# Kernel optimization log

Measured on AMD Instinct MI355X. Metric: run time of the kernel, lower is better.

Reference implementation:

```python
import jax, jax.numpy as jnp
import numpy as np

TEMPERATURE = 0.8
TOP_P = 0.9
NEG_INF = float('-inf')


def _top_k_filter(logits, k):
    # keep only the top-k logits per row; mask the rest to -inf.
    # torch.topk + scatter mask == threshold at the k-th largest value (ties measure-zero for float logits)
    kth = jax.lax.top_k(logits, k)[0][..., -1:]  # [B, 1]
    return jnp.where(logits < kth, NEG_INF, logits)


def _top_p_filter(logits, p):
    # nucleus filtering: sort desc, cumulative softmax mass, drop tail past p (always keep the top token)
    B, V = logits.shape
    order = jnp.argsort(-logits, axis=-1)                       # [B, V] descending order
    sorted_logits = jnp.take_along_axis(logits, order, axis=-1)
    cdf = jnp.cumsum(jax.nn.softmax(sorted_logits, axis=-1), axis=-1)
    remove_sorted = cdf > p
    remove_sorted = jnp.roll(remove_sorted, 1, axis=-1).at[..., 0].set(False)  # shift so first token crossing p is kept
    rows = jnp.arange(B)[:, None]
    remove = jnp.zeros((B, V), dtype=bool).at[rows, order].set(remove_sorted)  # scatter back to original positions
    return jnp.where(remove, NEG_INF, logits)


def _sample_multinomial(probs, key):
    # inverse-CDF sampling: idx = #{cumsum <= r}
    r = jax.random.uniform(key, (probs.shape[0], 1), dtype=probs.dtype)
    cdf = jnp.cumsum(probs, axis=-1)
    return jnp.sum(cdf <= r, axis=-1, keepdims=True)  # [B, 1] int


def setup_inputs() -> dict:
    key = jax.random.key(0)
    logits = jax.random.normal(key, (256, 50257), dtype=jnp.float32) * 4.0
    return {"logits": logits, "top_k": 50}


def reference(logits, top_k):
    logits = logits / TEMPERATURE
    logits = _top_k_filter(logits, top_k)
    logits = _top_p_filter(logits, TOP_P)
    probs = jax.nn.softmax(logits, axis=-1)
    next_ids = _sample_multinomial(probs, jax.random.fold_in(jax.random.key(0), 1))
    return next_ids
```

## Files before the change

### kernel.cpp

```cpp
#include <hip/hip_runtime.h>
#include <stdint.h>


#define BLOCK 512
#define BINS  4096
#define CAP   1024
#define TOPP  0.9f

__device__ __forceinline__ unsigned orderKey(float x) {
  unsigned u = __float_as_uint(x);
  return (u & 0x80000000u) ? ~u : (u | 0x80000000u);
}

__device__ __forceinline__ void threefry2x32(unsigned k0, unsigned k1,
                                             unsigned x0, unsigned x1,
                                             unsigned &o0, unsigned &o1) {
  unsigned k2 = k0 ^ k1 ^ 0x1BD11BDAu;
  x0 += k0; x1 += k1;
#define TFR(rr) { x0 += x1; x1 = (x1 << (rr)) | (x1 >> (32 - (rr))); x1 ^= x0; }
  TFR(13) TFR(15) TFR(26) TFR(6)
  x0 += k1; x1 += k2 + 1u;
  TFR(17) TFR(29) TFR(16) TFR(24)
  x0 += k2; x1 += k0 + 2u;
  TFR(13) TFR(15) TFR(26) TFR(6)
  x0 += k0; x1 += k1 + 3u;
  TFR(17) TFR(29) TFR(16) TFR(24)
  x0 += k1; x1 += k2 + 4u;
  TFR(13) TFR(15) TFR(26) TFR(6)
  x0 += k2; x1 += k0 + 5u;
#undef TFR
  o0 = x0; o1 = x1;
}

__global__ __launch_bounds__(BLOCK) void Sampler_28845000360542_kernel(
    const float* __restrict__ logits, const int* __restrict__ topk_ptr,
    int* __restrict__ out, int V, int B) {
  __shared__ unsigned hist[BINS];
  __shared__ float    cval[CAP];
  __shared__ int      cidx[CAP];
  __shared__ float    sval[CAP];
  __shared__ int      sidx[CAP];
  __shared__ unsigned psum[BLOCK];
  __shared__ short    ord[CAP];
  __shared__ unsigned s_cnt;
  __shared__ int      s_binLo;
  __shared__ int      s_ns;
  __shared__ int      s_K;
  __shared__ float    s_S2;
  __shared__ float    s_r;

  const int tid = threadIdx.x;
  const int row = blockIdx.x;
  const float* __restrict__ rp = logits + (size_t)row * (size_t)V;
  const float4* __restrict__ rp4 = (const float4*)rp;
  const int V4 = V >> 2;

  int k = topk_ptr[0];
  if (k < 1) k = 1;
  if (k > V) k = V;

  for (int i = tid; i < BINS; i += BLOCK) hist[i] = 0u;
  if (tid == 0) s_cnt = 0u;
  __syncthreads();

  for (int i = tid; i < V4; i += BLOCK) {
    float4 v = rp4[i];
    atomicAdd(&hist[orderKey(v.x) >> 20], 1u);
    atomicAdd(&hist[orderKey(v.y) >> 20], 1u);
    atomicAdd(&hist[orderKey(v.z) >> 20], 1u);
    atomicAdd(&hist[orderKey(v.w) >> 20], 1u);
  }
  for (int i = (V4 << 2) + tid; i < V; i += BLOCK)
    atomicAdd(&hist[orderKey(rp[i]) >> 20], 1u);
  __syncthreads();

  {
    const int C = BINS / BLOCK;
    unsigned s = 0;
#pragma unroll
    for (int j = 0; j < C; ++j) s += hist[tid * C + j];
    psum[tid] = s;
  }
  __syncthreads();

  if (tid == 0) {
    const int C = BINS / BLOCK;
    unsigned cum = 0;
    int chunk = 0;
    for (int t = BLOCK - 1; t >= 0; --t) {
      if (cum + psum[t] >= (unsigned)k) { chunk = t; break; }
      cum += psum[t];
    }
    int bstar = chunk * C;
    for (int b = chunk * C + C - 1; b >= chunk * C; --b) {
      if (cum + hist[b] >= (unsigned)k) { bstar = b; break; }
      cum += hist[b];
    }
    unsigned nCol = cum + hist[bstar];
    int bLo = bstar;
    if (bstar > 0 && nCol + hist[bstar - 1] <= (unsigned)CAP) bLo = bstar - 1;
    s_binLo = bLo;
  }
  __syncthreads();

  const unsigned binLo = (unsigned)s_binLo;
  for (int i = tid; i < V4; i += BLOCK) {
    float4 v = rp4[i];
    float vv[4] = {v.x, v.y, v.z, v.w};
#pragma unroll
    for (int c = 0; c < 4; ++c) {
      if ((orderKey(vv[c]) >> 20) >= binLo) {
        unsigned pos = atomicAdd(&s_cnt, 1u);
        if (pos < CAP) { cval[pos] = vv[c]; cidx[pos] = (i << 2) + c; }
      }
    }
  }
  for (int i = (V4 << 2) + tid; i < V; i += BLOCK) {
    float x = rp[i];
    if ((orderKey(x) >> 20) >= binLo) {
      unsigned pos = atomicAdd(&s_cnt, 1u);
      if (pos < CAP) { cval[pos] = x; cidx[pos] = i; }
    }
  }
  __syncthreads();

  int n = (int)s_cnt;
  if (n > CAP) n = CAP;

  for (int i = tid; i < n; i += BLOCK) cval[i] = cval[i] / 0.8f;
  __syncthreads();
  for (int i = tid; i < n; i += BLOCK) {
    float v = cval[i];
    int   id = cidx[i];
    int   rk = 0;
    for (int j = 0; j < n; ++j) {
      float vj = cval[j];
      rk += (vj > v) || (vj == v && cidx[j] < id);
    }
    sval[rk] = v;
    sidx[rk] = id;
  }
  __syncthreads();

  if (tid == 0) {
    int ns = (n < k) ? n : k;
    float kv = sval[ns - 1];
    while (ns < n && sval[ns] == kv) ++ns;
    s_ns = ns;
  }
  __syncthreads();
  const int ns = s_ns;

  const float m = sval[0];
  for (int i = tid; i < ns; i += BLOCK) cval[i] = expf(sval[i] - m);
  __syncthreads();

  if (tid == 0) {
    float S = 0.f;
    for (int i = 0; i < ns; ++i) S += cval[i];
    float c = 0.f;
    int K = ns;
    for (int i = 0; i < ns; ++i) {
      if (i > 0 && c > TOPP) { K = i; break; }
      c += cval[i] / S;
    }
    float S2 = 0.f;
    for (int i = 0; i < K; ++i) S2 += cval[i];
    s_K = K;
    s_S2 = S2;

    unsigned kk0, kk1, o0, o1;
    threefry2x32(0u, 0u, 0u, 1u, kk0, kk1);
    threefry2x32(kk0, kk1, 0u, (unsigned)row, o0, o1);
    unsigned bits = o0 ^ o1;
    float r = __uint_as_float((bits >> 9) | 0x3F800000u) - 1.0f;
    s_r = (r < 0.f) ? 0.f : r;
    (void)B;
  }
  __syncthreads();
  const int K = s_K;

  for (int i = tid; i < K; i += BLOCK) {
    int id = sidx[i];
    int rk = 0;
    for (int j = 0; j < K; ++j) rk += (sidx[j] < id);
    ord[rk] = (short)i;
  }
  __syncthreads();

  if (tid == 0) {
    const float S2 = s_S2;
    const float rr = s_r;
    float c = 0.f;
    int ans = V;
    for (int t = 0; t < K; ++t) {
      int i = ord[t];
      c += cval[i] / S2;
      if (c > rr) { ans = sidx[i]; break; }
    }
    out[row] = ans;
  }
}

extern "C" void kernel_launch(void* const* d_in, const int* in_sizes, int n_in,
                              void* d_out, int out_size, void* d_ws, size_t ws_size,
                              hipStream_t stream) {
  const float* logits = (const float*)d_in[0];
  const int*   topk   = (const int*)d_in[1];
  int*         out    = (int*)d_out;
  const int B = out_size;
  const int V = in_sizes[0] / B;
  hipLaunchKernelGGL(Sampler_28845000360542_kernel, dim3(B), dim3(BLOCK), 0,
                     stream, logits, topk, out, V, B);
}
```

Before: 118.5 us.

## Split per-row sampler into multi-kernel pipeline with chunked histogram and collect

```diff
diff --git a/kernel.cpp b/kernel.cpp
--- a/kernel.cpp
+++ b/kernel.cpp
@@ -2,10 +2,12 @@
 #include <stdint.h>
 
 
-#define BLOCK 512
-#define BINS  4096
-#define CAP   1024
-#define TOPP  0.9f
+#define BINS     4096
+#define CAP      1024
+#define TOPP     0.9f
+#define S_CHUNKS 8
+#define HBLOCK   256
+#define TAILB    512
 
 __device__ __forceinline__ unsigned orderKey(float x) {
   unsigned u = __float_as_uint(x);
@@ -32,104 +34,154 @@
   o0 = x0; o1 = x1;
 }
 
-__global__ __launch_bounds__(BLOCK) void Sampler_28845000360542_kernel(
-    const float* __restrict__ logits, const int* __restrict__ topk_ptr,
-    int* __restrict__ out, int V, int B) {
+__global__ __launch_bounds__(256) void k_zero(unsigned* __restrict__ p, int n) {
+  int i = blockIdx.x * 256 + threadIdx.x;
+  int stride = gridDim.x * 256;
+  for (; i < n; i += stride) p[i] = 0u;
+}
+
+__global__ __launch_bounds__(HBLOCK) void k_hist(
+    const float* __restrict__ logits, unsigned* __restrict__ ghist, int V) {
   __shared__ unsigned hist[BINS];
-  __shared__ float    cval[CAP];
-  __shared__ int      cidx[CAP];
-  __shared__ float    sval[CAP];
-  __shared__ int      sidx[CAP];
-  __shared__ unsigned psum[BLOCK];
-  __shared__ short    ord[CAP];
-  __shared__ unsigned s_cnt;
-  __shared__ int      s_binLo;
-  __shared__ int      s_ns;
-  __shared__ int      s_K;
-  __shared__ float    s_S2;
-  __shared__ float    s_r;
-
-  const int tid = threadIdx.x;
-  const int row = blockIdx.x;
+  const int row = blockIdx.y, chunk = blockIdx.x, tid = threadIdx.x;
   const float* __restrict__ rp = logits + (size_t)row * (size_t)V;
   const float4* __restrict__ rp4 = (const float4*)rp;
   const int V4 = V >> 2;
-
-  int k = topk_ptr[0];
-  if (k < 1) k = 1;
-  if (k > V) k = V;
-
-  for (int i = tid; i < BINS; i += BLOCK) hist[i] = 0u;
-  if (tid == 0) s_cnt = 0u;
-  __syncthreads();
-
-  for (int i = tid; i < V4; i += BLOCK) {
+  const int beg = (int)((long long)chunk * V4 / S_CHUNKS);
+  const int end = (int)((long long)(chunk + 1) * V4 / S_CHUNKS);
+
+  for (int i = tid; i < BINS; i += HBLOCK) hist[i] = 0u;
+  __syncthreads();
+
+  for (int i = beg + tid; i < end; i += HBLOCK) {
     float4 v = rp4[i];
     atomicAdd(&hist[orderKey(v.x) >> 20], 1u);
     atomicAdd(&hist[orderKey(v.y) >> 20], 1u);
     atomicAdd(&hist[orderKey(v.z) >> 20], 1u);
     atomicAdd(&hist[orderKey(v.w) >> 20], 1u);
   }
-  for (int i = (V4 << 2) + tid; i < V; i += BLOCK)
-    atomicAdd(&hist[orderKey(rp[i]) >> 20], 1u);
-  __syncthreads();
-
-  {
-    const int C = BINS / BLOCK;
-    unsigned s = 0;
+  if (chunk == S_CHUNKS - 1) {
+    for (int i = (V4 << 2) + tid; i < V; i += HBLOCK)
+      atomicAdd(&hist[orderKey(rp[i]) >> 20], 1u);
+  }
+  __syncthreads();
+
+  unsigned* __restrict__ gh = ghist + (size_t)row * BINS;
+  for (int i = tid; i < BINS; i += HBLOCK) {
+    unsigned c = hist[i];
+    if (c) atomicAdd(&gh[i], c);
+  }
+}
+
+__global__ __launch_bounds__(256) void k_select(
+    const unsigned* __restrict__ ghist, const int* __restrict__ topk_ptr,
+    int* __restrict__ binLoArr, int V) {
+  __shared__ unsigned hist[BINS];
+  __shared__ unsigned psum[256];
+  const int row = blockIdx.x, tid = threadIdx.x;
+  const unsigned* __restrict__ gh = ghist + (size_t)row * BINS;
+  for (int i = tid; i < BINS; i += 256) hist[i] = gh[i];
+  __syncthreads();
+
+  int k = topk_ptr[0];
+  if (k < 1) k = 1;
+  if (k > V) k = V;
+
+  const int C = BINS / 256;
+  unsigned s = 0;
 #pragma unroll
-    for (int j = 0; j < C; ++j) s += hist[tid * C + j];
-    psum[tid] = s;
-  }
-  __syncthreads();
-
-  if (tid == 0) {
-    const int C = BINS / BLOCK;
+  for (int j = 0; j < C; ++j) s += hist[tid * C + j];
+  psum[tid] = s;
+  __syncthreads();
+
+  if (tid == 0) {
     unsigned cum = 0;
-    int chunk = 0;
-    for (int t = BLOCK - 1; t >= 0; --t) {
-      if (cum + psum[t] >= (unsigned)k) { chunk = t; break; }
+    int ch = 0;
+    for (int t = 255; t >= 0; --t) {
+      if (cum + psum[t] >= (unsigned)k) { ch = t; break; }
       cum += psum[t];
     }
-    int bstar = chunk * C;
-    for (int b = chunk * C + C - 1; b >= chunk * C; --b) {
+    int bstar = ch * C;
+    for (int b = ch * C + C - 1; b >= ch * C; --b) {
       if (cum + hist[b] >= (unsigned)k) { bstar = b; break; }
       cum += hist[b];
     }
     unsigned nCol = cum + hist[bstar];
     int bLo = bstar;
     if (bstar > 0 && nCol + hist[bstar - 1] <= (unsigned)CAP) bLo = bstar - 1;
-    s_binLo = bLo;
-  }
-  __syncthreads();
-
-  const unsigned binLo = (unsigned)s_binLo;
-  for (int i = tid; i < V4; i += BLOCK) {
+    binLoArr[row] = bLo;
+  }
+}
+
+__global__ __launch_bounds__(HBLOCK) void k_collect(
+    const float* __restrict__ logits, const int* __restrict__ binLoArr,
+    unsigned* __restrict__ cnt, float* __restrict__ cvalg,
+    int* __restrict__ cidxg, int V) {
+  const int row = blockIdx.y, chunk = blockIdx.x, tid = threadIdx.x;
+  const unsigned binLo = (unsigned)binLoArr[row];
+  const float* __restrict__ rp = logits + (size_t)row * (size_t)V;
+  const float4* __restrict__ rp4 = (const float4*)rp;
+  const int V4 = V >> 2;
+  const int beg = (int)((long long)chunk * V4 / S_CHUNKS);
+  const int end = (int)((long long)(chunk + 1) * V4 / S_CHUNKS);
+  float* __restrict__ cv = cvalg + (size_t)row * CAP;
+  int*   __restrict__ ci = cidxg + (size_t)row * CAP;
+
+  for (int i = beg + tid; i < end; i += HBLOCK) {
     float4 v = rp4[i];
     float vv[4] = {v.x, v.y, v.z, v.w};
 #pragma unroll
     for (int c = 0; c < 4; ++c) {
       if ((orderKey(vv[c]) >> 20) >= binLo) {
-        unsigned pos = atomicAdd(&s_cnt, 1u);
-        if (pos < CAP) { cval[pos] = vv[c]; cidx[pos] = (i << 2) + c; }
+        unsigned pos = atomicAdd(&cnt[row], 1u);
+        if (pos < CAP) { cv[pos] = vv[c]; ci[pos] = (i << 2) + c; }
       }
     }
   }
-  for (int i = (V4 << 2) + tid; i < V; i += BLOCK) {
-    float x = rp[i];
-    if ((orderKey(x) >> 20) >= binLo) {
-      unsigned pos = atomicAdd(&s_cnt, 1u);
-      if (pos < CAP) { cval[pos] = x; cidx[pos] = i; }
-    }
-  }
-  __syncthreads();
-
-  int n = (int)s_cnt;
+  if (chunk == S_CHUNKS - 1) {
+    for (int i = (V4 << 2) + tid; i < V; i += HBLOCK) {
+      float x = rp[i];
+      if ((orderKey(x) >> 20) >= binLo) {
+        unsigned pos = atomicAdd(&cnt[row], 1u);
+        if (pos < CAP) { cv[pos] = x; ci[pos] = i; }
+      }
+    }
+  }
+}
+
+__global__ __launch_bounds__(TAILB) void k_tail(
+    const unsigned* __restrict__ cnt, const float* __restrict__ cvalg,
+    const int* __restrict__ cidxg, const int* __restrict__ topk_ptr,
+    int* __restrict__ out, int V) {
+  __shared__ float cval[CAP];
+  __shared__ int   cidx[CAP];
+  __shared__ float sval[CAP];
+  __shared__ int   sidx[CAP];
+  __shared__ short ord[CAP];
+  __shared__ int   s_ns;
+  __shared__ int   s_K;
+  __shared__ float s_S2;
+  __shared__ float s_r;
+
+  const int tid = threadIdx.x;
+  const int row = blockIdx.x;
+
+  int k = topk_ptr[0];
+  if (k < 1) k = 1;
+  if (k > V) k = V;
+
+  int n = (int)cnt[row];
   if (n > CAP) n = CAP;
 
-  for (int i = tid; i < n; i += BLOCK) cval[i] = cval[i] / 0.8f;
-  __syncthreads();
-  for (int i = tid; i < n; i += BLOCK) {
+  const float* __restrict__ cv = cvalg + (size_t)row * CAP;
+  const int*   __restrict__ ci = cidxg + (size_t)row * CAP;
+  for (int i = tid; i < n; i += TAILB) {
+    cval[i] = cv[i] / 0.8f;
+    cidx[i] = ci[i];
+  }
+  __syncthreads();
+
+  for (int i = tid; i < n; i += TAILB) {
     float v = cval[i];
     int   id = cidx[i];
     int   rk = 0;
@@ -152,7 +204,7 @@
   const int ns = s_ns;
 
   const float m = sval[0];
-  for (int i = tid; i < ns; i += BLOCK) cval[i] = expf(sval[i] - m);
+  for (int i = tid; i < ns; i += TAILB) cval[i] = expf(sval[i] - m);
   __syncthreads();
 
   if (tid == 0) {
@@ -175,12 +227,11 @@
     unsigned bits = o0 ^ o1;
     float r = __uint_as_float((bits >> 9) | 0x3F800000u) - 1.0f;
     s_r = (r < 0.f) ? 0.f : r;
-    (void)B;
   }
   __syncthreads();
   const int K = s_K;
 
-  for (int i = tid; i < K; i += BLOCK) {
+  for (int i = tid; i < K; i += TAILB) {
     int id = sidx[i];
     int rk = 0;
     for (int j = 0; j < K; ++j) rk += (sidx[j] < id);
@@ -210,6 +261,24 @@
   int*         out    = (int*)d_out;
   const int B = out_size;
   const int V = in_sizes[0] / B;
-  hipLaunchKernelGGL(Sampler_28845000360542_kernel, dim3(B), dim3(BLOCK), 0,
-                     stream, logits, topk, out, V, B);
-}
+
+  char* ws = (char*)d_ws;
+  unsigned* ghist  = (unsigned*)ws;
+  unsigned* cnt    = (unsigned*)(ws + (size_t)B * BINS * 4);
+  int*      binLo  = (int*)(ws + (size_t)B * BINS * 4 + B * 4);
+  float*    cvalg  = (float*)(ws + (size_t)B * BINS * 4 + B * 8);
+  int*      cidxg  = (int*)(ws + (size_t)B * BINS * 4 + B * 8 +
+                            (size_t)B * CAP * 4);
+
+  const int nzero = B * BINS + B;
+  hipLaunchKernelGGL(k_zero, dim3((nzero + 255) / 256), dim3(256), 0, stream,
+                     ghist, nzero);
+  hipLaunchKernelGGL(k_hist, dim3(S_CHUNKS, B), dim3(HBLOCK), 0, stream,
+                     logits, ghist, V);
+  hipLaunchKernelGGL(k_select, dim3(B), dim3(256), 0, stream,
+                     ghist, topk, binLo, V);
+  hipLaunchKernelGGL(k_collect, dim3(S_CHUNKS, B), dim3(HBLOCK), 0, stream,
+                     logits, binLo, cnt, cvalg, cidxg, V);
+  hipLaunchKernelGGL(k_tail, dim3(B), dim3(TAILB), 0, stream,
+                     cnt, cvalg, cidxg, topk, out, V);
+}
```

Result: slower. 160.6 us (+35.6%).

## Split each row across eight blocks with per-chunk candidate selection and merge kernel

Applied to the files above, without the earlier changes.

```diff
diff --git a/kernel.cpp b/kernel.cpp
--- a/kernel.cpp
+++ b/kernel.cpp
@@ -2,10 +2,13 @@
 #include <stdint.h>
 
 
-#define BLOCK 512
-#define BINS  4096
-#define CAP   1024
-#define TOPP  0.9f
+#define BINS     4096
+#define S_CHUNKS 8
+#define PB       256
+#define SEG      256
+#define CAPT     (S_CHUNKS * SEG)
+#define TB       512
+#define TOPP     0.9f
 
 __device__ __forceinline__ unsigned orderKey(float x) {
   unsigned u = __float_as_uint(x);
@@ -32,140 +35,222 @@
   o0 = x0; o1 = x1;
 }
 
-__global__ __launch_bounds__(BLOCK) void Sampler_28845000360542_kernel(
+__global__ __launch_bounds__(PB) void k_pass1(
     const float* __restrict__ logits, const int* __restrict__ topk_ptr,
-    int* __restrict__ out, int V, int B) {
+    int* __restrict__ scnt, float* __restrict__ svals, int* __restrict__ sidxs,
+    int V) {
   __shared__ unsigned hist[BINS];
-  __shared__ float    cval[CAP];
-  __shared__ int      cidx[CAP];
-  __shared__ float    sval[CAP];
-  __shared__ int      sidx[CAP];
-  __shared__ unsigned psum[BLOCK];
-  __shared__ short    ord[CAP];
-  __shared__ unsigned s_cnt;
-  __shared__ int      s_binLo;
-  __shared__ int      s_ns;
-  __shared__ int      s_K;
-  __shared__ float    s_S2;
-  __shared__ float    s_r;
-
-  const int tid = threadIdx.x;
-  const int row = blockIdx.x;
+  __shared__ unsigned psum[PB];
+  __shared__ float    lval[SEG];
+  __shared__ int      lidx[SEG];
+  __shared__ unsigned lcnt;
+  __shared__ int      s_b;
+
+  const int row = blockIdx.y, chunk = blockIdx.x, tid = threadIdx.x;
   const float* __restrict__ rp = logits + (size_t)row * (size_t)V;
   const float4* __restrict__ rp4 = (const float4*)rp;
   const int V4 = V >> 2;
-
-  int k = topk_ptr[0];
-  if (k < 1) k = 1;
-  if (k > V) k = V;
-
-  for (int i = tid; i < BINS; i += BLOCK) hist[i] = 0u;
-  if (tid == 0) s_cnt = 0u;
-  __syncthreads();
-
-  for (int i = tid; i < V4; i += BLOCK) {
+  const int beg = (int)((long long)chunk * V4 / S_CHUNKS);
+  const int end = (int)((long long)(chunk + 1) * V4 / S_CHUNKS);
+  const bool last = (chunk == S_CHUNKS - 1);
+  const int rembeg = V4 << 2;
+
+  for (int i = tid; i < BINS; i += PB) hist[i] = 0u;
+  if (tid == 0) lcnt = 0u;
+  __syncthreads();
+
+  for (int i = beg + tid; i < end; i += PB) {
     float4 v = rp4[i];
     atomicAdd(&hist[orderKey(v.x) >> 20], 1u);
     atomicAdd(&hist[orderKey(v.y) >> 20], 1u);
     atomicAdd(&hist[orderKey(v.z) >> 20], 1u);
     atomicAdd(&hist[orderKey(v.w) >> 20], 1u);
   }
-  for (int i = (V4 << 2) + tid; i < V; i += BLOCK)
-    atomicAdd(&hist[orderKey(rp[i]) >> 20], 1u);
-  __syncthreads();
-
+  if (last)
+    for (int i = rembeg + tid; i < V; i += PB)
+      atomicAdd(&hist[orderKey(rp[i]) >> 20], 1u);
+  __syncthreads();
+
+  int k = topk_ptr[0];
+  if (k < 1) k = 1;
+  if (k > V) k = V;
+  const int ec = (end - beg) * 4 + (last ? (V - rembeg) : 0);
+  if (k > ec) k = ec;
+
+  const int C = BINS / PB;
   {
-    const int C = BINS / BLOCK;
     unsigned s = 0;
 #pragma unroll
     for (int j = 0; j < C; ++j) s += hist[tid * C + j];
     psum[tid] = s;
   }
   __syncthreads();
-
-  if (tid == 0) {
-    const int C = BINS / BLOCK;
+  if (tid == 0) {
     unsigned cum = 0;
-    int chunk = 0;
-    for (int t = BLOCK - 1; t >= 0; --t) {
-      if (cum + psum[t] >= (unsigned)k) { chunk = t; break; }
+    int ch = 0;
+    for (int t = PB - 1; t >= 0; --t) {
+      if (cum + psum[t] >= (unsigned)k) { ch = t; break; }
       cum += psum[t];
     }
-    int bstar = chunk * C;
-    for (int b = chunk * C + C - 1; b >= chunk * C; --b) {
+    int bstar = ch * C;
+    for (int b = ch * C + C - 1; b >= ch * C; --b) {
       if (cum + hist[b] >= (unsigned)k) { bstar = b; break; }
       cum += hist[b];
     }
-    unsigned nCol = cum + hist[bstar];
-    int bLo = bstar;
-    if (bstar > 0 && nCol + hist[bstar - 1] <= (unsigned)CAP) bLo = bstar - 1;
-    s_binLo = bLo;
-  }
-  __syncthreads();
-
-  const unsigned binLo = (unsigned)s_binLo;
-  for (int i = tid; i < V4; i += BLOCK) {
+    s_b = (bstar > 0) ? bstar - 1 : 0;
+  }
+  __syncthreads();
+
+  const unsigned bLo = (unsigned)s_b;
+  for (int i = beg + tid; i < end; i += PB) {
     float4 v = rp4[i];
     float vv[4] = {v.x, v.y, v.z, v.w};
 #pragma unroll
     for (int c = 0; c < 4; ++c) {
-      if ((orderKey(vv[c]) >> 20) >= binLo) {
-        unsigned pos = atomicAdd(&s_cnt, 1u);
-        if (pos < CAP) { cval[pos] = vv[c]; cidx[pos] = (i << 2) + c; }
+      if ((orderKey(vv[c]) >> 20) >= bLo) {
+        unsigned pos = atomicAdd(&lcnt, 1u);
+        if (pos < SEG) { lval[pos] = vv[c]; lidx[pos] = (i << 2) + c; }
       }
     }
   }
-  for (int i = (V4 << 2) + tid; i < V; i += BLOCK) {
-    float x = rp[i];
-    if ((orderKey(x) >> 20) >= binLo) {
-      unsigned pos = atomicAdd(&s_cnt, 1u);
-      if (pos < CAP) { cval[pos] = x; cidx[pos] = i; }
-    }
-  }
-  __syncthreads();
-
-  int n = (int)s_cnt;
-  if (n > CAP) n = CAP;
-
-  for (int i = tid; i < n; i += BLOCK) cval[i] = cval[i] / 0.8f;
-  __syncthreads();
-  for (int i = tid; i < n; i += BLOCK) {
-    float v = cval[i];
-    int   id = cidx[i];
+  if (last)
+    for (int i = rembeg + tid; i < V; i += PB) {
+      float x = rp[i];
+      if ((orderKey(x) >> 20) >= bLo) {
+        unsigned pos = atomicAdd(&lcnt, 1u);
+        if (pos < SEG) { lval[pos] = x; lidx[pos] = i; }
+      }
+    }
+  __syncthreads();
+
+  int n = (lcnt > SEG) ? SEG : (int)lcnt;
+  const int sb = row * S_CHUNKS + chunk;
+  if (tid == 0) scnt[sb] = n;
+  float* __restrict__ ov = svals + (size_t)sb * SEG;
+  int*   __restrict__ oi = sidxs + (size_t)sb * SEG;
+  for (int i = tid; i < n; i += PB) { ov[i] = lval[i]; oi[i] = lidx[i]; }
+}
+
+__global__ __launch_bounds__(TB) void k_tail(
+    const int* __restrict__ scnt, const float* __restrict__ svals,
+    const int* __restrict__ sidxs, const int* __restrict__ topk_ptr,
+    int* __restrict__ out, int V) {
+  __shared__ float    cval[CAPT];
+  __shared__ int      cidx[CAPT];
+  __shared__ float    sval[CAPT];
+  __shared__ int      sidx[CAPT];
+  __shared__ short    ord[CAPT];
+  __shared__ unsigned hist[BINS];
+  __shared__ unsigned psum[TB];
+  __shared__ int      s_off[S_CHUNKS + 1];
+  __shared__ unsigned s_mc;
+  __shared__ int      s_bg, s_ns, s_K;
+  __shared__ float    s_S2, s_r;
+
+  const int row = blockIdx.x, tid = threadIdx.x;
+  int k = topk_ptr[0];
+  if (k < 1) k = 1;
+  if (k > V) k = V;
+
+  if (tid == 0) {
+    int off = 0;
+    for (int c = 0; c < S_CHUNKS; ++c) { s_off[c] = off; off += scnt[row * S_CHUNKS + c]; }
+    s_off[S_CHUNKS] = off;
+    s_mc = 0u;
+  }
+  for (int i = tid; i < BINS; i += TB) hist[i] = 0u;
+  __syncthreads();
+
+  const int n = s_off[S_CHUNKS];
+  for (int c = 0; c < S_CHUNKS; ++c) {
+    const int cn = s_off[c + 1] - s_off[c];
+    const int o  = s_off[c];
+    const float* __restrict__ sv = svals + (size_t)(row * S_CHUNKS + c) * SEG;
+    const int*   __restrict__ si = sidxs + (size_t)(row * S_CHUNKS + c) * SEG;
+    for (int i = tid; i < cn; i += TB) {
+      float x = sv[i];
+      cval[o + i] = x;
+      cidx[o + i] = si[i];
+      atomicAdd(&hist[orderKey(x) >> 20], 1u);
+    }
+  }
+  __syncthreads();
+
+  const int kk = (k > n) ? n : k;
+  {
+    const int C = BINS / TB;
+    unsigned s = 0;
+#pragma unroll
+    for (int j = 0; j < C; ++j) s += hist[tid * C + j];
+    psum[tid] = s;
+  }
+  __syncthreads();
+  if (tid == 0) {
+    const int C = BINS / TB;
+    unsigned cum = 0;
+    int ch = 0;
+    for (int t = TB - 1; t >= 0; --t) {
+      if (cum + psum[t] >= (unsigned)kk) { ch = t; break; }
+      cum += psum[t];
+    }
+    int bstar = ch * C;
+    for (int b = ch * C + C - 1; b >= ch * C; --b) {
+      if (cum + hist[b] >= (unsigned)kk) { bstar = b; break; }
+      cum += hist[b];
+    }
+    s_bg = (bstar > 0) ? bstar - 1 : 0;
+  }
+  __syncthreads();
+
+  const unsigned bg = (unsigned)s_bg;
+  for (int i = tid; i < n; i += TB) {
+    float x = cval[i];
+    if ((orderKey(x) >> 20) >= bg) {
+      unsigned pos = atomicAdd(&s_mc, 1u);
+      sval[pos] = x / 0.8f;
+      sidx[pos] = cidx[i];
+    }
+  }
+  __syncthreads();
+  const int m = (int)s_mc;
+
+  for (int i = tid; i < m; i += TB) {
+    float v = sval[i];
+    int   id = sidx[i];
     int   rk = 0;
-    for (int j = 0; j < n; ++j) {
-      float vj = cval[j];
-      rk += (vj > v) || (vj == v && cidx[j] < id);
-    }
-    sval[rk] = v;
-    sidx[rk] = id;
-  }
-  __syncthreads();
-
-  if (tid == 0) {
-    int ns = (n < k) ? n : k;
-    float kv = sval[ns - 1];
-    while (ns < n && sval[ns] == kv) ++ns;
+    for (int j = 0; j < m; ++j) {
+      float vj = sval[j];
+      rk += (vj > v) || (vj == v && sidx[j] < id);
+    }
+    cval[rk] = v;
+    cidx[rk] = id;
+  }
+  __syncthreads();
+
+  if (tid == 0) {
+    int ns = (m < kk) ? m : kk;
+    float kv = cval[ns - 1];
+    while (ns < m && cval[ns] == kv) ++ns;
     s_ns = ns;
   }
   __syncthreads();
   const int ns = s_ns;
 
-  const float m = sval[0];
-  for (int i = tid; i < ns; i += BLOCK) cval[i] = expf(sval[i] - m);
+  const float mx = cval[0];
+  for (int i = tid; i < ns; i += TB) sval[i] = expf(cval[i] - mx);
   __syncthreads();
 
   if (tid == 0) {
     float S = 0.f;
-    for (int i = 0; i < ns; ++i) S += cval[i];
+    for (int i = 0; i < ns; ++i) S += sval[i];
     float c = 0.f;
     int K = ns;
     for (int i = 0; i < ns; ++i) {
       if (i > 0 && c > TOPP) { K = i; break; }
-      c += cval[i] / S;
+      c += sval[i] / S;
     }
     float S2 = 0.f;
-    for (int i = 0; i < K; ++i) S2 += cval[i];
+    for (int i = 0; i < K; ++i) S2 += sval[i];
     s_K = K;
     s_S2 = S2;
 
@@ -175,15 +260,14 @@
     unsigned bits = o0 ^ o1;
     float r = __uint_as_float((bits >> 9) | 0x3F800000u) - 1.0f;
     s_r = (r < 0.f) ? 0.f : r;
-    (void)B;
   }
   __syncthreads();
   const int K = s_K;
 
-  for (int i = tid; i < K; i += BLOCK) {
-    int id = sidx[i];
+  for (int i = tid; i < K; i += TB) {
+    int id = cidx[i];
     int rk = 0;
-    for (int j = 0; j < K; ++j) rk += (sidx[j] < id);
+    for (int j = 0; j < K; ++j) rk += (cidx[j] < id);
     ord[rk] = (short)i;
   }
   __syncthreads();
@@ -195,8 +279,8 @@
     int ans = V;
     for (int t = 0; t < K; ++t) {
       int i = ord[t];
-      c += cval[i] / S2;
-      if (c > rr) { ans = sidx[i]; break; }
+      c += sval[i] / S2;
+      if (c > rr) { ans = cidx[i]; break; }
     }
     out[row] = ans;
   }
@@ -210,6 +294,15 @@
   int*         out    = (int*)d_out;
   const int B = out_size;
   const int V = in_sizes[0] / B;
-  hipLaunchKernelGGL(Sampler_28845000360542_kernel, dim3(B), dim3(BLOCK), 0,
-                     stream, logits, topk, out, V, B);
-}
+
+  char* ws = (char*)d_ws;
+  int*   scnt  = (int*)ws;
+  float* svals = (float*)(ws + (size_t)B * S_CHUNKS * 4);
+  int*   sidxs = (int*)(ws + (size_t)B * S_CHUNKS * 4 +
+                        (size_t)B * S_CHUNKS * SEG * 4);
+
+  hipLaunchKernelGGL(k_pass1, dim3(S_CHUNKS, B), dim3(PB), 0, stream,
+                     logits, topk, scnt, svals, sidxs, V);
+  hipLaunchKernelGGL(k_tail, dim3(B), dim3(TB), 0, stream,
+                     scnt, svals, sidxs, topk, out, V);
+}
```

Result: slower. 135.3 us (+14.2%).

## Single-pass fixed-threshold prefilter with wave-level top-k selection and fallback path

Applied to the files above, without the earlier changes.

```diff
diff --git a/kernel.cpp b/kernel.cpp
--- a/kernel.cpp
+++ b/kernel.cpp
@@ -2,10 +2,13 @@
 #include <stdint.h>
 
 
-#define BLOCK 512
-#define BINS  4096
-#define CAP   1024
-#define TOPP  0.9f
+#define BLOCK  1024
+#define CAPN   2048
+#define SLOTS  (CAPN / 64)
+#define WCAP   256
+#define TOPP   0.9f
+#define TOPT_F 8.0f
+#define OK8    0xC1000000u
 
 __device__ __forceinline__ unsigned orderKey(float x) {
   unsigned u = __float_as_uint(x);
@@ -32,24 +35,23 @@
   o0 = x0; o1 = x1;
 }
 
-__global__ __launch_bounds__(BLOCK) void Sampler_28845000360542_kernel(
+__global__ __launch_bounds__(BLOCK) void k_all(
     const float* __restrict__ logits, const int* __restrict__ topk_ptr,
-    int* __restrict__ out, int V, int B) {
-  __shared__ unsigned hist[BINS];
-  __shared__ float    cval[CAP];
-  __shared__ int      cidx[CAP];
-  __shared__ float    sval[CAP];
-  __shared__ int      sidx[CAP];
-  __shared__ unsigned psum[BLOCK];
-  __shared__ short    ord[CAP];
-  __shared__ unsigned s_cnt;
-  __shared__ int      s_binLo;
-  __shared__ int      s_ns;
-  __shared__ int      s_K;
-  __shared__ float    s_S2;
-  __shared__ float    s_r;
-
-  const int tid = threadIdx.x;
+    int* __restrict__ out, int V) {
+  __shared__ float    bufv[CAPN];
+  __shared__ int      bufi[CAPN];
+  __shared__ float    wv[WCAP];
+  __shared__ int      wi[WCAP];
+  __shared__ float    sv[WCAP];
+  __shared__ int      si[WCAP];
+  __shared__ float    evl[WCAP];
+  __shared__ short    ordl[WCAP];
+  __shared__ unsigned lcnt, wcnt;
+  __shared__ int      s_slow, s_tot;
+  __shared__ unsigned s_thr;
+  __shared__ int      redc[BLOCK / 64];
+
+  const int tid = threadIdx.x, lane = tid & 63, wid = tid >> 6;
   const int row = blockIdx.x;
   const float* __restrict__ rp = logits + (size_t)row * (size_t)V;
   const float4* __restrict__ rp4 = (const float4*)rp;
@@ -59,144 +61,218 @@
   if (k < 1) k = 1;
   if (k > V) k = V;
 
-  for (int i = tid; i < BINS; i += BLOCK) hist[i] = 0u;
-  if (tid == 0) s_cnt = 0u;
+  if (tid == 0) { lcnt = 0u; wcnt = 0u; }
   __syncthreads();
 
-  for (int i = tid; i < V4; i += BLOCK) {
-    float4 v = rp4[i];
-    atomicAdd(&hist[orderKey(v.x) >> 20], 1u);
-    atomicAdd(&hist[orderKey(v.y) >> 20], 1u);
-    atomicAdd(&hist[orderKey(v.z) >> 20], 1u);
-    atomicAdd(&hist[orderKey(v.w) >> 20], 1u);
-  }
-  for (int i = (V4 << 2) + tid; i < V; i += BLOCK)
-    atomicAdd(&hist[orderKey(rp[i]) >> 20], 1u);
+#define PUSH(v_, idx_) do {                                             \
+    bool q_ = (v_) >= TOPT_F;                                           \
+    unsigned long long m_ = __ballot(q_);                               \
+    if (q_) {                                                           \
+      int ldr_ = __ffsll((unsigned long long)m_) - 1;                   \
+      unsigned base_;                                                   \
+      if (lane == ldr_) base_ = atomicAdd(&lcnt, (unsigned)__popcll(m_)); \
+      base_ = __shfl(base_, ldr_);                                      \
+      unsigned p_ = base_ + (unsigned)__popcll(m_ & ((1ull << lane) - 1ull)); \
+      if (p_ < CAPN) { bufv[p_] = (v_); bufi[p_] = (idx_); }            \
+    } } while (0)
+
+  const int V4m = V4 & ~(4 * BLOCK - 1);
+  for (int base = 0; base < V4m; base += 4 * BLOCK) {
+    const int i0 = base + tid;
+    float4 a = rp4[i0];
+    float4 b = rp4[i0 + BLOCK];
+    float4 c = rp4[i0 + 2 * BLOCK];
+    float4 d = rp4[i0 + 3 * BLOCK];
+    PUSH(a.x, (i0 << 2));                PUSH(a.y, (i0 << 2) + 1);
+    PUSH(a.z, (i0 << 2) + 2);            PUSH(a.w, (i0 << 2) + 3);
+    PUSH(b.x, ((i0 + BLOCK) << 2));      PUSH(b.y, ((i0 + BLOCK) << 2) + 1);
+    PUSH(b.z, ((i0 + BLOCK) << 2) + 2);  PUSH(b.w, ((i0 + BLOCK) << 2) + 3);
+    PUSH(c.x, ((i0 + 2 * BLOCK) << 2));     PUSH(c.y, ((i0 + 2 * BLOCK) << 2) + 1);
+    PUSH(c.z, ((i0 + 2 * BLOCK) << 2) + 2); PUSH(c.w, ((i0 + 2 * BLOCK) << 2) + 3);
+    PUSH(d.x, ((i0 + 3 * BLOCK) << 2));     PUSH(d.y, ((i0 + 3 * BLOCK) << 2) + 1);
+    PUSH(d.z, ((i0 + 3 * BLOCK) << 2) + 2); PUSH(d.w, ((i0 + 3 * BLOCK) << 2) + 3);
+  }
+  for (int i = V4m + tid; i < V4; i += BLOCK) {
+    float4 a = rp4[i];
+    PUSH(a.x, (i << 2));     PUSH(a.y, (i << 2) + 1);
+    PUSH(a.z, (i << 2) + 2); PUSH(a.w, (i << 2) + 3);
+  }
+  for (int i = (V4 << 2) + tid; i < V; i += BLOCK) PUSH(rp[i], i);
+#undef PUSH
   __syncthreads();
 
-  {
-    const int C = BINS / BLOCK;
-    unsigned s = 0;
-#pragma unroll
-    for (int j = 0; j < C; ++j) s += hist[tid * C + j];
-    psum[tid] = s;
+  if (wid == 0) {
+    const int n = ((int)lcnt > CAPN) ? CAPN : (int)lcnt;
+    unsigned key[SLOTS];
+#pragma unroll
+    for (int s = 0; s < SLOTS; ++s) {
+      int i = lane + (s << 6);
+      key[s] = (i < n) ? orderKey(bufv[i]) : 0u;
+    }
+    bool ok = (lcnt <= (unsigned)CAPN) && (n >= k);
+    unsigned kraw = 0u;
+    if (ok) {
+      unsigned lo = 1u, hi = 0xFFFFFFFFu;
+      while (lo < hi) {
+        unsigned mid = lo + ((hi - lo + 1u) >> 1);
+        int c = 0;
+#pragma unroll
+        for (int s = 0; s < SLOTS; ++s)
+          if ((s << 6) < n) c += __popcll(__ballot(key[s] >= mid));
+        if (c >= k) lo = mid; else hi = mid - 1u;
+      }
+      kraw = lo;
+      ok = (kraw >= OK8 + 4u);
+    }
+    if (lane == 0) { s_slow = ok ? 0 : 1; s_thr = ok ? (kraw - 4u) : 0u; }
   }
   __syncthreads();
 
-  if (tid == 0) {
-    const int C = BINS / BLOCK;
-    unsigned cum = 0;
-    int chunk = 0;
-    for (int t = BLOCK - 1; t >= 0; --t) {
-      if (cum + psum[t] >= (unsigned)k) { chunk = t; break; }
-      cum += psum[t];
-    }
-    int bstar = chunk * C;
-    for (int b = chunk * C + C - 1; b >= chunk * C; --b) {
-      if (cum + hist[b] >= (unsigned)k) { bstar = b; break; }
-      cum += hist[b];
-    }
-    unsigned nCol = cum + hist[bstar];
-    int bLo = bstar;
-    if (bstar > 0 && nCol + hist[bstar - 1] <= (unsigned)CAP) bLo = bstar - 1;
-    s_binLo = bLo;
-  }
-  __syncthreads();
-
-  const unsigned binLo = (unsigned)s_binLo;
-  for (int i = tid; i < V4; i += BLOCK) {
-    float4 v = rp4[i];
-    float vv[4] = {v.x, v.y, v.z, v.w};
-#pragma unroll
-    for (int c = 0; c < 4; ++c) {
-      if ((orderKey(vv[c]) >> 20) >= binLo) {
-        unsigned pos = atomicAdd(&s_cnt, 1u);
-        if (pos < CAP) { cval[pos] = vv[c]; cidx[pos] = (i << 2) + c; }
+  if (s_slow) {
+    unsigned lo = 1u, hi = 0xFFFFFFFFu;
+    while (lo < hi) {
+      unsigned mid = lo + ((hi - lo + 1u) >> 1);
+      int c = 0;
+      for (int i = tid; i < V; i += BLOCK) c += (orderKey(rp[i]) >= mid);
+      for (int o = 32; o; o >>= 1) c += __shfl_down(c, o);
+      if (lane == 0) redc[wid] = c;
+      __syncthreads();
+      if (tid == 0) {
+        int t = 0;
+        for (int w = 0; w < BLOCK / 64; ++w) t += redc[w];
+        s_tot = t;
       }
-    }
-  }
-  for (int i = (V4 << 2) + tid; i < V; i += BLOCK) {
-    float x = rp[i];
-    if ((orderKey(x) >> 20) >= binLo) {
-      unsigned pos = atomicAdd(&s_cnt, 1u);
-      if (pos < CAP) { cval[pos] = x; cidx[pos] = i; }
-    }
-  }
-  __syncthreads();
-
-  int n = (int)s_cnt;
-  if (n > CAP) n = CAP;
-
-  for (int i = tid; i < n; i += BLOCK) cval[i] = cval[i] / 0.8f;
-  __syncthreads();
-  for (int i = tid; i < n; i += BLOCK) {
-    float v = cval[i];
-    int   id = cidx[i];
+      __syncthreads();
+      if (s_tot >= k) lo = mid; else hi = mid - 1u;
+      __syncthreads();
+    }
+    if (tid == 0) { lcnt = 0u; s_thr = (lo >= 5u) ? lo - 4u : 1u; }
+    __syncthreads();
+    const unsigned thr = s_thr;
+    for (int i = tid; i < V; i += BLOCK) {
+      float x = rp[i];
+      if (orderKey(x) >= thr) {
+        unsigned p = atomicAdd(&lcnt, 1u);
+        if (p < CAPN) { bufv[p] = x; bufi[p] = i; }
+      }
+    }
+    __syncthreads();
+  }
+
+  if (wid != 0) return;
+
+  const int n = ((int)lcnt > CAPN) ? CAPN : (int)lcnt;
+  const unsigned thr = s_thr;
+
+  for (int i = lane; i < n; i += 64) {
+    float x = bufv[i];
+    if (orderKey(x) >= thr) {
+      unsigned p = atomicAdd(&wcnt, 1u);
+      if (p < WCAP) { wv[p] = x / 0.8f; wi[p] = bufi[i]; }
+    }
+  }
+  int m = (int)wcnt;
+  if (m > WCAP) m = WCAP;
+  if (m == 0) { if (lane == 0) out[row] = V; return; }
+
+  unsigned skey[WCAP / 64];
+#pragma unroll
+  for (int s = 0; s < WCAP / 64; ++s) {
+    int i = lane + (s << 6);
+    skey[s] = (i < m) ? orderKey(wv[i]) : 0u;
+  }
+  const int kk = (k < m) ? k : m;
+  unsigned lo = 1u, hi = 0xFFFFFFFFu;
+  while (lo < hi) {
+    unsigned mid = lo + ((hi - lo + 1u) >> 1);
+    int c = 0;
+#pragma unroll
+    for (int s = 0; s < WCAP / 64; ++s)
+      c += __popcll(__ballot(skey[s] >= mid));
+    if (c >= kk) lo = mid; else hi = mid - 1u;
+  }
+  const unsigned kvs = lo;
+  int ns = 0;
+#pragma unroll
+  for (int s = 0; s < WCAP / 64; ++s)
+    ns += __popcll(__ballot(skey[s] >= kvs));
+
+  for (int i = lane; i < m; i += 64) {
+    float v = wv[i];
+    int   id = wi[i];
     int   rk = 0;
-    for (int j = 0; j < n; ++j) {
-      float vj = cval[j];
-      rk += (vj > v) || (vj == v && cidx[j] < id);
-    }
-    sval[rk] = v;
-    sidx[rk] = id;
-  }
-  __syncthreads();
-
-  if (tid == 0) {
-    int ns = (n < k) ? n : k;
-    float kv = sval[ns - 1];
-    while (ns < n && sval[ns] == kv) ++ns;
-    s_ns = ns;
-  }
-  __syncthreads();
-  const int ns = s_ns;
-
-  const float m = sval[0];
-  for (int i = tid; i < ns; i += BLOCK) cval[i] = expf(sval[i] - m);
-  __syncthreads();
-
-  if (tid == 0) {
+    for (int j = 0; j < m; ++j) {
+      float vj = wv[j];
+      rk += (vj > v) || (vj == v && wi[j] < id);
+    }
+    sv[rk] = v;
+    si[rk] = id;
+  }
+
+  unsigned tk0, tk1, o0, o1;
+  threefry2x32(0u, 0u, 0u, 1u, tk0, tk1);
+  threefry2x32(tk0, tk1, 0u, (unsigned)row, o0, o1);
+  unsigned bits = o0 ^ o1;
+  float r0 = __uint_as_float((bits >> 9) | 0x3F800000u) - 1.0f;
+  const float rr = (r0 < 0.f) ? 0.f : r0;
+
+  if (ns <= 64) {
+    float myv  = (lane < ns) ? sv[lane] : 0.f;
+    int   myid = (lane < ns) ? si[lane] : 0x7FFFFFFF;
+    const float mx = __shfl(myv, 0);
+    float mye = (lane < ns) ? expf(myv - mx) : 0.f;
+
     float S = 0.f;
-    for (int i = 0; i < ns; ++i) S += cval[i];
+    for (int i = 0; i < ns; ++i) S += __shfl(mye, i);
     float c = 0.f;
     int K = ns;
     for (int i = 0; i < ns; ++i) {
       if (i > 0 && c > TOPP) { K = i; break; }
-      c += cval[i] / S;
+      c += __shfl(mye, i) / S;
     }
     float S2 = 0.f;
-    for (int i = 0; i < K; ++i) S2 += cval[i];
-    s_K = K;
-    s_S2 = S2;
-
-    unsigned kk0, kk1, o0, o1;
-    threefry2x32(0u, 0u, 0u, 1u, kk0, kk1);
-    threefry2x32(kk0, kk1, 0u, (unsigned)row, o0, o1);
-    unsigned bits = o0 ^ o1;
-    float r = __uint_as_float((bits >> 9) | 0x3F800000u) - 1.0f;
-    s_r = (r < 0.f) ? 0.f : r;
-    (void)B;
-  }
-  __syncthreads();
-  const int K = s_K;
-
-  for (int i = tid; i < K; i += BLOCK) {
-    int id = sidx[i];
+    for (int i = 0; i < K; ++i) S2 += __shfl(mye, i);
+
     int rk = 0;
-    for (int j = 0; j < K; ++j) rk += (sidx[j] < id);
-    ord[rk] = (short)i;
-  }
-  __syncthreads();
-
-  if (tid == 0) {
-    const float S2 = s_S2;
-    const float rr = s_r;
-    float c = 0.f;
+    for (int j = 0; j < K; ++j) {
+      int idj = __shfl(myid, j);
+      rk += (idj < myid);
+    }
+    float c2 = 0.f;
     int ans = V;
     for (int t = 0; t < K; ++t) {
-      int i = ord[t];
-      c += cval[i] / S2;
-      if (c > rr) { ans = sidx[i]; break; }
+      unsigned long long mm = __ballot((lane < K) && (rk == t));
+      int src = __ffsll((unsigned long long)mm) - 1;
+      c2 += __shfl(mye, src) / S2;
+      if (c2 > rr) { ans = __shfl(myid, src); break; }
+    }
+    if (lane == 0) out[row] = ans;
+    return;
+  }
+
+  for (int i = lane; i < ns; i += 64) evl[i] = expf(sv[i] - sv[0]);
+  if (lane == 0) {
+    float S = 0.f;
+    for (int i = 0; i < ns; ++i) S += evl[i];
+    float c = 0.f;
+    int K = ns;
+    for (int i = 0; i < ns; ++i) {
+      if (i > 0 && c > TOPP) { K = i; break; }
+      c += evl[i] / S;
+    }
+    float S2 = 0.f;
+    for (int i = 0; i < K; ++i) S2 += evl[i];
+    for (int i = 0; i < K; ++i) {
+      int id = si[i], rk2 = 0;
+      for (int j = 0; j < K; ++j) rk2 += (si[j] < id);
+      ordl[rk2] = (short)i;
+    }
+    float c2 = 0.f;
+    int ans = V;
+    for (int t = 0; t < K; ++t) {
+      int i = ordl[t];
+      c2 += evl[i] / S2;
+      if (c2 > rr) { ans = si[i]; break; }
     }
     out[row] = ans;
   }
@@ -210,6 +286,7 @@
   int*         out    = (int*)d_out;
   const int B = out_size;
   const int V = in_sizes[0] / B;
-  hipLaunchKernelGGL(Sampler_28845000360542_kernel, dim3(B), dim3(BLOCK), 0,
-                     stream, logits, topk, out, V, B);
-}
+  (void)d_ws; (void)ws_size; (void)n_in;
+  hipLaunchKernelGGL(k_all, dim3(B), dim3(BLOCK), 0, stream,
+                     logits, topk, out, V);
+}
```

Measured after the change: 120.9 us. 2.0% more time.
